# Kernel optimization log

Measured on AMD Instinct MI355X. Metric: run time of the kernel, lower is better.

## Reference

```python
import jax, jax.numpy as jnp
import numpy as np

D_MODEL = 1024
NUM_HEADS = 16
D_K = D_MODEL // NUM_HEADS
SCALE = float(np.sqrt(D_K))


def setup_inputs() -> dict:
    key = jax.random.key(0)
    ks = jax.random.split(key, 11)
    B, S, D = 2, 2048, D_MODEL
    def lin(kw):
        # xavier-uniform-ish weight, zero bias (matches torch init style)
        lim = float(np.sqrt(6.0 / (D + D)))
        return jax.random.uniform(kw, (D, D), jnp.float32, -lim, lim)
    return {
        "q": jax.random.normal(ks[0], (B, S, D), jnp.float32),
        "k": jax.random.normal(ks[1], (B, S, D), jnp.float32),
        "v": jax.random.normal(ks[2], (B, S, D), jnp.float32),
        "Wq": lin(ks[3]), "bq": jnp.zeros((D,), jnp.float32),
        "Wk": lin(ks[4]), "bk": jnp.zeros((D,), jnp.float32),
        "Wv": lin(ks[5]), "bv": jnp.zeros((D,), jnp.float32),
        "Wo": lin(ks[6]), "bo": jnp.zeros((D,), jnp.float32),
    }


def _split_heads(x):
    B, S, _ = x.shape
    return x.reshape(B, S, NUM_HEADS, D_K).transpose(0, 2, 1, 3)  # (B,H,S,dk)


def reference(q, k, v, Wq, bq, Wk, bk, Wv, bv, Wo, bo):
    # torch nn.Linear: y = x @ W.T + b
    Q = _split_heads(q @ Wq.T + bq)
    K = _split_heads(k @ Wk.T + bk)
    V = _split_heads(v @ Wv.T + bv)
    scores = jnp.einsum("bhqd,bhkd->bhqk", Q, K) / SCALE
    # numerically-stable softmax with detached max (as in the torch code)
    m = jax.lax.stop_gradient(jnp.max(scores, axis=-1, keepdims=True))
    exp_scores = jnp.exp(scores - m)
    attn = exp_scores / (jnp.sum(exp_scores, axis=-1, keepdims=True) + 1e-9)
    out = jnp.einsum("bhqk,bhkd->bhqd", attn, V)  # (B,H,S,dk)
    B, H, S, dk = out.shape
    out = out.transpose(0, 2, 1, 3).reshape(B, S, H * dk)
    return out @ Wo.T + bo
```

## Files before the change

kernel.cpp:

```cpp
#include <hip/hip_runtime.h>


#define D_MODEL 1024
#define NHEADS  16
#define DKH     64
#define SEQ     2048
#define BATCH   2
#define MTOT    (BATCH * SEQ)
#define XE      ((long)MTOT * D_MODEL)
#define WE      ((long)D_MODEL * D_MODEL)
#define QSCALE  0.18033688011112042f

typedef __attribute__((ext_vector_type(8))) short short8v;
typedef __attribute__((ext_vector_type(4))) short short4v;
typedef __attribute__((ext_vector_type(4))) float f32x4;

typedef __attribute__((address_space(1))) void as1_void;
typedef __attribute__((address_space(3))) void as3_void;

__device__ __forceinline__ void gload16(const void* g, void* l) {
    __builtin_amdgcn_global_load_lds((const as1_void*)g, (as3_void*)l, 16, 0, 0);
}

__device__ __forceinline__ unsigned short f2bf(float x) {
    unsigned int u = __float_as_uint(x);
    u += 0x7FFFu + ((u >> 16) & 1u);
    return (unsigned short)(u >> 16);
}

__device__ __forceinline__ float fexp2(float x) {
    return __builtin_amdgcn_exp2f(x);
}

__device__ __forceinline__ unsigned int cvt_pk_bf16(float lo, float hi) {
    unsigned int r;
    asm("v_cvt_pk_bf16_f32 %0, %1, %2" : "=v"(r) : "v"(lo), "v"(hi));
    return r;
}

__device__ __forceinline__ int swz_u(int row, int col) {
    int byte = (col << 1) ^ ((row & 7) << 4);
    return (row << 6) + (byte >> 1);
}

__device__ __forceinline__ int swz_v(int d, int kv) {
    int slot = (d & 6) | ((d >> 3) & 1);
    int byte = (kv << 1) ^ (slot << 4);
    return (d << 6) + (byte >> 1);
}

struct ConvArgs {
    const float*    src[7];
    unsigned short* dst[7];
    int             n4[7];
};

__global__ __launch_bounds__(256) void convert_kernel(ConvArgs a) {
    int z = blockIdx.y;
    const float4*   s = (const float4*)a.src[z];
    unsigned short* d = a.dst[z];
    int n = a.n4[z];
    for (int i = blockIdx.x * blockDim.x + threadIdx.x; i < n;
         i += gridDim.x * blockDim.x) {
        float4 v = s[i];
        ushort4 o;
        o.x = f2bf(v.x); o.y = f2bf(v.y); o.z = f2bf(v.z); o.w = f2bf(v.w);
        *(ushort4*)(d + 4L * i) = o;
    }
}

#define PBM 256
#define PBK 64
#define PTILE (PBM * PBK)

__global__ __launch_bounds__(512) void proj_kernel(
    const unsigned short* __restrict__ xb, const unsigned short* __restrict__ wb,
    const float* __restrict__ bq, const float* __restrict__ bk,
    const float* __restrict__ bv, unsigned short* __restrict__ qkv) {
    __shared__ unsigned short As[2 * PTILE];
    __shared__ unsigned short Bs[2 * PTILE];

    const int t    = threadIdx.x;
    const int lane = t & 63;
    const int w    = t >> 6;
    const int wm   = w >> 2, wn = w & 3;
    const int l15  = lane & 15, g = lane >> 4;

    const int bid = blockIdx.x;
    const int xcd = bid & 7;
    const int k   = bid >> 3;
    const int ty  = (xcd << 1) | (k & 1);
    const int tx  = (k >> 1) & 3;
    const int z   = k >> 3;
    const float* bias = (z == 0) ? bq : (z == 1) ? bk : bv;
    const float scale = (z == 0) ? QSCALE : 1.0f;

    const unsigned short* A  = xb + (long)z * XE;
    const unsigned short* Bm = wb + (long)z * WE;
    unsigned short*       C  = qkv + (long)z * XE;
    const long m0 = (long)ty * PBM;
    const long n0 = (long)tx * PBM;
    const int  K  = D_MODEL;

    f32x4 acc[8][4] = {};

    int srow[4], scol[4];
#pragma unroll
    for (int c = 0; c < 4; ++c) {
        int idx = t + c * 512;
        srow[c] = idx >> 3;
        scol[c] = ((idx & 7) ^ (srow[c] & 7)) * 8;
    }

#define PSTAGE(k0, buf)                                                    \
    _Pragma("unroll")                                                      \
    for (int c = 0; c < 4; ++c) {                                          \
        int idx = t + c * 512;                                             \
        gload16(A  + (m0 + srow[c]) * K + (k0) + scol[c],                  \
                &As[(buf) * PTILE + idx * 8]);                             \
        gload16(Bm + (n0 + srow[c]) * K + (k0) + scol[c],                  \
                &Bs[(buf) * PTILE + idx * 8]);                             \
    }

    PSTAGE(0, 0);
    int cur = 0;

    for (int it = 0; it < K / PBK; ++it) {
        const int nxt = cur ^ 1;
        const int kn  = ((it + 1) * PBK) & (K - 1);
        PSTAGE(kn, nxt);
        asm volatile("s_waitcnt vmcnt(8)" ::: "memory");
        asm volatile("s_waitcnt lgkmcnt(0)" ::: "memory");
        __builtin_amdgcn_sched_barrier(0);
        __builtin_amdgcn_s_barrier();
        __builtin_amdgcn_sched_barrier(0);

        const unsigned short* Ab = &As[cur * PTILE];
        const unsigned short* Bb = &Bs[cur * PTILE];

#pragma unroll
        for (int kk = 0; kk < 2; ++kk) {
            short8v bf_[4];
#pragma unroll
            for (int nf = 0; nf < 4; ++nf) {
                int r = wn * 64 + nf * 16 + l15;
                bf_[nf] = *(const short8v*)&Bb[r * 64 + (((kk * 4 + g) ^ (r & 7)) * 8)];
            }
#pragma unroll
            for (int mh = 0; mh < 2; ++mh) {
                short8v af_[4];
#pragma unroll
                for (int i = 0; i < 4; ++i) {
                    int r = wm * 128 + (mh * 4 + i) * 16 + l15;
                    af_[i] = *(const short8v*)&Ab[r * 64 + (((kk * 4 + g) ^ (r & 7)) * 8)];
                }
                __builtin_amdgcn_s_setprio(1);
#pragma unroll
                for (int i = 0; i < 4; ++i)
#pragma unroll
                    for (int nf = 0; nf < 4; ++nf)
                        acc[mh * 4 + i][nf] = __builtin_amdgcn_mfma_f32_16x16x32_bf16(
                            af_[i], bf_[nf], acc[mh * 4 + i][nf], 0, 0, 0);
                __builtin_amdgcn_s_setprio(0);
            }
        }

        asm volatile("s_waitcnt lgkmcnt(0)" ::: "memory");
        __builtin_amdgcn_sched_barrier(0);
        __builtin_amdgcn_s_barrier();
        __builtin_amdgcn_sched_barrier(0);
        cur = nxt;
    }

    float bvv[4];
#pragma unroll
    for (int nf = 0; nf < 4; ++nf)
        bvv[nf] = bias[n0 + wn * 64 + nf * 16 + l15];

#pragma unroll
    for (int mf = 0; mf < 8; ++mf)
#pragma unroll
        for (int nf = 0; nf < 4; ++nf)
#pragma unroll
            for (int r = 0; r < 4; ++r) {
                long row = m0 + wm * 128 + mf * 16 + g * 4 + r;
                long col = n0 + wn * 64 + nf * 16 + l15;
                C[row * (long)D_MODEL + col] =
                    f2bf((acc[mf][nf][r] + bvv[nf]) * scale);
            }
#undef PSTAGE
}

__global__ __launch_bounds__(256) void out_kernel(
    const unsigned short* __restrict__ ob, const unsigned short* __restrict__ wo,
    const float* __restrict__ bo, float* __restrict__ out) {
    __shared__ unsigned short As[128 * 32];
    __shared__ unsigned short Bs[128 * 32];

    const int t    = threadIdx.x;
    const int lane = t & 63;
    const int w    = t >> 6;
    const int wm   = w >> 1, wn = w & 1;
    const int l15  = lane & 15, g = lane >> 4;

    const int bid = blockIdx.x;
    const int xcd = bid & 7;
    const int k   = bid >> 3;
    const long m0 = (long)((xcd << 2) | (k & 3)) * 128;
    const long n0 = (long)(k >> 2) * 128;
    const int  K  = D_MODEL, N = D_MODEL;

    f32x4 acc[4][4] = {};

    const int idx0 = t, idx1 = t + 256;
    const int r0 = idx0 >> 2, c0 = (idx0 & 3) * 8;
    const int r1 = idx1 >> 2, c1 = (idx1 & 3) * 8;
    const unsigned short* pa0 = ob + (m0 + r0) * K + c0;
    const unsigned short* pa1 = ob + (m0 + r1) * K + c1;
    const unsigned short* pb0 = wo + (n0 + r0) * K + c0;
    const unsigned short* pb1 = wo + (n0 + r1) * K + c1;

    for (int k0 = 0; k0 < K; k0 += 32) {
        gload16(pa0 + k0, &As[idx0 * 8]);
        gload16(pa1 + k0, &As[idx1 * 8]);
        gload16(pb0 + k0, &Bs[idx0 * 8]);
        gload16(pb1 + k0, &Bs[idx1 * 8]);
        __syncthreads();

        short8v af[4], bf_[4];
#pragma unroll
        for (int mf = 0; mf < 4; ++mf)
            af[mf] = *(const short8v*)&As[(wm * 64 + mf * 16 + l15) * 32 + g * 8];
#pragma unroll
        for (int nf = 0; nf < 4; ++nf)
            bf_[nf] = *(const short8v*)&Bs[(wn * 64 + nf * 16 + l15) * 32 + g * 8];
#pragma unroll
        for (int mf = 0; mf < 4; ++mf)
#pragma unroll
            for (int nf = 0; nf < 4; ++nf)
                acc[mf][nf] = __builtin_amdgcn_mfma_f32_16x16x32_bf16(
                    af[mf], bf_[nf], acc[mf][nf], 0, 0, 0);
        __syncthreads();
    }

    float bvv[4];
#pragma unroll
    for (int nf = 0; nf < 4; ++nf)
        bvv[nf] = bo[n0 + wn * 64 + nf * 16 + l15];

#pragma unroll
    for (int mf = 0; mf < 4; ++mf)
#pragma unroll
        for (int nf = 0; nf < 4; ++nf)
#pragma unroll
            for (int r = 0; r < 4; ++r) {
                long row = m0 + wm * 64 + mf * 16 + g * 4 + r;
                long col = n0 + wn * 64 + nf * 16 + l15;
                out[row * (long)N + col] = acc[mf][nf][r] + bvv[nf];
            }
}

#define KVB 4096

__global__ __launch_bounds__(512) void attn_kernel(
    const unsigned short* __restrict__ Qb, const unsigned short* __restrict__ Kb,
    const unsigned short* __restrict__ Vb, unsigned short* __restrict__ Ob) {
    __shared__ alignas(16) unsigned short Ks[2 * KVB];
    __shared__ alignas(16) unsigned short Vt[2 * KVB];
    __shared__ alignas(16) unsigned short Ps[8][16 * 64];
    __shared__ alignas(16) float corrS[8][16];

    const int t = threadIdx.x, lane = t & 63, w = t >> 6;
    const int l15 = lane & 15, g = lane >> 4;
    const int bid = blockIdx.x;
    const int xcd = bid & 7;
    const int kk2 = bid >> 3;
    const int bh  = (xcd << 2) | (kk2 & 3);
    const int qb  = kk2 >> 2;
    const long headoff = (long)(bh >> 4) * SEQ * D_MODEL + (long)(bh & 15) * DKH;
    const int q0w = qb * 128 + w * 16;

    short8v qf[2];
#pragma unroll
    for (int ks = 0; ks < 2; ++ks)
        qf[ks] = *(const short8v*)(Qb + headoff +
            (long)(q0w + l15) * D_MODEL + ks * 32 + g * 8);

    short8v onesv;
#pragma unroll
    for (int j = 0; j < 8; ++j) onesv[j] = (short)0x3F80;

    f32x4 o[4] = {};
    f32x4 ol = {};
    float mrun = -3.0e38f;

    const int vd0  = (t & 31) * 2;
    const int vkv0 = (t >> 5) * 4;
    const int kr0 = t >> 3, ks0 = t & 7;

    unsigned int va[4];

#define ISSUE_V(kt)                                                        \
    _Pragma("unroll")                                                      \
    for (int j = 0; j < 4; ++j)                                            \
        va[j] = *(const unsigned int*)(Vb + headoff +                      \
            (long)((kt) + vkv0 + j) * D_MODEL + vd0);

#define ISSUE_K(kt, off)                                                   \
    gload16(Kb + headoff + (long)((kt) + kr0) * D_MODEL +                  \
                ((ks0 ^ (kr0 & 7)) << 3), &Ks[(off) + t * 8]);

#define WRITE_V(off)                                                       \
    {                                                                      \
        short4v ra, rb;                                                    \
        _Pragma("unroll")                                                  \
        for (int j = 0; j < 4; ++j) {                                      \
            ra[j] = (short)(va[j] & 0xffffu);                              \
            rb[j] = (short)(va[j] >> 16);                                  \
        }                                                                  \
        *(short4v*)&Vt[(off) + swz_v(vd0,     vkv0)] = ra;                 \
        *(short4v*)&Vt[(off) + swz_v(vd0 + 1, vkv0)] = rb;                 \
    }

    asm volatile("s_waitcnt vmcnt(0)" ::: "memory");
    ISSUE_V(0);
    ISSUE_K(0, 0);
    WRITE_V(0);
    int cur = 0;

    for (int it = 0; it < SEQ / 64; ++it) {
        const int nxt = cur ^ 1;
        const int ktn = (((it + 1) & (SEQ / 64 - 1))) * 64;
        ISSUE_V(ktn);
        ISSUE_K(ktn, nxt * KVB);
        asm volatile("s_waitcnt vmcnt(5)" ::: "memory");
        asm volatile("s_waitcnt lgkmcnt(0)" ::: "memory");
        __builtin_amdgcn_sched_barrier(0);
        __builtin_amdgcn_s_barrier();
        __builtin_amdgcn_sched_barrier(0);

        const int kO = cur * KVB;

        f32x4 st[4] = {};
        __builtin_amdgcn_s_setprio(1);
#pragma unroll
        for (int ks = 0; ks < 2; ++ks)
#pragma unroll
            for (int mf = 0; mf < 4; ++mf) {
                short8v kf = *(const short8v*)&Ks[kO + swz_u(mf * 16 + l15, ks * 32 + g * 8)];
                st[mf] = __builtin_amdgcn_mfma_f32_16x16x32_bf16(
                    kf, qf[ks], st[mf], 0, 0, 0);
            }
        __builtin_amdgcn_s_setprio(0);

        float vmax = st[0][0];
#pragma unroll
        for (int mf = 0; mf < 4; ++mf)
#pragma unroll
            for (int r = 0; r < 4; ++r)
                vmax = fmaxf(vmax, st[mf][r]);
        vmax = fmaxf(vmax, __shfl_xor(vmax, 16));
        vmax = fmaxf(vmax, __shfl_xor(vmax, 32));

        const bool grow = __any(vmax > mrun + 8.0f);
        if (grow) {
            float mnew = fmaxf(mrun, vmax);
            float corr = fexp2(mrun - mnew);
            mrun = mnew;
            if (g == 0) corrS[w][l15] = corr;
        }

#pragma unroll
        for (int mf = 0; mf < 4; ++mf)
#pragma unroll
            for (int r = 0; r < 4; ++r)
                st[mf][r] = fexp2(st[mf][r] - mrun);

        unsigned short* Pw = Ps[w];
#pragma unroll
        for (int mf = 0; mf < 4; ++mf) {
            uint2 pk;
            pk.x = cvt_pk_bf16(st[mf][0], st[mf][1]);
            pk.y = cvt_pk_bf16(st[mf][2], st[mf][3]);
            *(uint2*)&Pw[swz_u(l15, mf * 16 + g * 4)] = pk;
        }

        if (grow) {
            float4 cv = *(const float4*)&corrS[w][g * 4];
#pragma unroll
            for (int nd = 0; nd < 4; ++nd)
#pragma unroll
                for (int r = 0; r < 4; ++r)
                    o[nd][r] *= cv[r];
#pragma unroll
            for (int r = 0; r < 4; ++r) ol[r] *= cv[r];
        }

        __builtin_amdgcn_s_setprio(1);
#pragma unroll
        for (int ks2 = 0; ks2 < 2; ++ks2) {
            short8v pf = *(const short8v*)&Pw[swz_u(l15, ks2 * 32 + g * 8)];
            ol = __builtin_amdgcn_mfma_f32_16x16x32_bf16(
                pf, onesv, ol, 0, 0, 0);
#pragma unroll
            for (int nd = 0; nd < 4; ++nd) {
                short8v vf = *(const short8v*)&Vt[kO + swz_v(nd * 16 + l15, ks2 * 32 + g * 8)];
                o[nd] = __builtin_amdgcn_mfma_f32_16x16x32_bf16(
                    pf, vf, o[nd], 0, 0, 0);
            }
        }
        __builtin_amdgcn_s_setprio(0);

        WRITE_V(nxt * KVB);
        cur = nxt;
    }

#pragma unroll
    for (int r = 0; r < 4; ++r) {
        float inv = 1.f / (ol[r] + 1e-9f);
        long rowoff = headoff + (long)(q0w + g * 4 + r) * D_MODEL;
#pragma unroll
        for (int nd = 0; nd < 4; ++nd)
            Ob[rowoff + nd * 16 + l15] = f2bf(o[nd][r] * inv);
    }
#undef ISSUE_V
#undef ISSUE_K
#undef WRITE_V
}

extern "C" void kernel_launch(void* const* d_in, const int* in_sizes, int n_in,
                              void* d_out, int out_size, void* d_ws, size_t ws_size,
                              hipStream_t stream) {
    unsigned short* ws  = (unsigned short*)d_ws;
    unsigned short* xb  = ws;
    unsigned short* wb  = ws + 3L * XE;
    unsigned short* qkv = ws + 3L * XE + 4L * WE;
    unsigned short* ob  = qkv + 3L * XE;

    ConvArgs ca;
    ca.src[0] = (const float*)d_in[0]; ca.dst[0] = xb;           ca.n4[0] = (int)(XE / 4);
    ca.src[1] = (const float*)d_in[1]; ca.dst[1] = xb + XE;      ca.n4[1] = (int)(XE / 4);
    ca.src[2] = (const float*)d_in[2]; ca.dst[2] = xb + 2L * XE; ca.n4[2] = (int)(XE / 4);
    ca.src[3] = (const float*)d_in[3]; ca.dst[3] = wb;           ca.n4[3] = (int)(WE / 4);
    ca.src[4] = (const float*)d_in[5]; ca.dst[4] = wb + WE;      ca.n4[4] = (int)(WE / 4);
    ca.src[5] = (const float*)d_in[7]; ca.dst[5] = wb + 2L * WE; ca.n4[5] = (int)(WE / 4);
    ca.src[6] = (const float*)d_in[9]; ca.dst[6] = wb + 3L * WE; ca.n4[6] = (int)(WE / 4);

    hipLaunchKernelGGL(convert_kernel, dim3(512, 7), dim3(256), 0, stream, ca);

    hipLaunchKernelGGL(proj_kernel, dim3(192), dim3(512), 0, stream,
                       xb, wb, (const float*)d_in[4], (const float*)d_in[6],
                       (const float*)d_in[8], qkv);

    hipLaunchKernelGGL(attn_kernel, dim3(512), dim3(512), 0, stream,
                       qkv, qkv + XE, qkv + 2L * XE, ob);

    hipLaunchKernelGGL(out_kernel, dim3(256), dim3(256), 0, stream,
                       ob, wb + 3L * WE, (const float*)d_in[10], (float*)d_out);
}
```

Measured before the change: 132.7 us.

## Fuse fp32-to-bf16 activation conversion into projection GEMM staging

The projection kernel now reads the fp32 q/k/v activations directly, converts them to bf16 in registers and stores them to shared memory. This replaces the separate conversion pass over the three activation tensors, which wrote a bf16 copy to the workspace. The separate pass shrinks to weight conversion only. In exchange, the A-tile loads go through registers instead of async global-to-LDS loads, which doubles the A-side bytes read per tile and adds register pressure and load latency inside the main loop. The vmcnt wait is lowered to match the smaller number of async loads.

```diff
diff --git a/kernel.cpp b/kernel.cpp
--- a/kernel.cpp
+++ b/kernel.cpp
@@ -50,9 +50,9 @@
 }
 
 struct ConvArgs {
-    const float*    src[7];
-    unsigned short* dst[7];
-    int             n4[7];
+    const float*    src[4];
+    unsigned short* dst[4];
+    int             n4[4];
 };
 
 __global__ __launch_bounds__(256) void convert_kernel(ConvArgs a) {
@@ -74,7 +74,8 @@
 #define PTILE (PBM * PBK)
 
 __global__ __launch_bounds__(512) void proj_kernel(
-    const unsigned short* __restrict__ xb, const unsigned short* __restrict__ wb,
+    const float* __restrict__ xq, const float* __restrict__ xk,
+    const float* __restrict__ xv, const unsigned short* __restrict__ wb,
     const float* __restrict__ bq, const float* __restrict__ bk,
     const float* __restrict__ bv, unsigned short* __restrict__ qkv) {
     __shared__ unsigned short As[2 * PTILE];
@@ -95,7 +96,7 @@
     const float* bias = (z == 0) ? bq : (z == 1) ? bk : bv;
     const float scale = (z == 0) ? QSCALE : 1.0f;
 
-    const unsigned short* A  = xb + (long)z * XE;
+    const float* Af = (z == 0) ? xq : (z == 1) ? xk : xv;
     const unsigned short* Bm = wb + (long)z * WE;
     unsigned short*       C  = qkv + (long)z * XE;
     const long m0 = (long)ty * PBM;
@@ -113,13 +114,30 @@
     }
 
 #define PSTAGE(k0, buf)                                                    \
-    _Pragma("unroll")                                                      \
-    for (int c = 0; c < 4; ++c) {                                          \
-        int idx = t + c * 512;                                             \
-        gload16(A  + (m0 + srow[c]) * K + (k0) + scol[c],                  \
-                &As[(buf) * PTILE + idx * 8]);                             \
-        gload16(Bm + (n0 + srow[c]) * K + (k0) + scol[c],                  \
-                &Bs[(buf) * PTILE + idx * 8]);                             \
+    {                                                                      \
+        float4 a0_[4], a1_[4];                                             \
+        _Pragma("unroll")                                                  \
+        for (int c = 0; c < 4; ++c) {                                      \
+            const float* src = Af + (m0 + srow[c]) * K + (k0) + scol[c];   \
+            a0_[c] = *(const float4*)(src);                                \
+            a1_[c] = *(const float4*)(src + 4);                            \
+        }                                                                  \
+        _Pragma("unroll")                                                  \
+        for (int c = 0; c < 4; ++c) {                                      \
+            int idx = t + c * 512;                                         \
+            gload16(Bm + (n0 + srow[c]) * K + (k0) + scol[c],              \
+                    &Bs[(buf) * PTILE + idx * 8]);                         \
+        }                                                                  \
+        _Pragma("unroll")                                                  \
+        for (int c = 0; c < 4; ++c) {                                      \
+            int idx = t + c * 512;                                         \
+            uint4 pk;                                                      \
+            pk.x = cvt_pk_bf16(a0_[c].x, a0_[c].y);                        \
+            pk.y = cvt_pk_bf16(a0_[c].z, a0_[c].w);                        \
+            pk.z = cvt_pk_bf16(a1_[c].x, a1_[c].y);                        \
+            pk.w = cvt_pk_bf16(a1_[c].z, a1_[c].w);                        \
+            *(uint4*)&As[(buf) * PTILE + idx * 8] = pk;                    \
+        }                                                                  \
     }
 
     PSTAGE(0, 0);
@@ -129,7 +147,7 @@
         const int nxt = cur ^ 1;
         const int kn  = ((it + 1) * PBK) & (K - 1);
         PSTAGE(kn, nxt);
-        asm volatile("s_waitcnt vmcnt(8)" ::: "memory");
+        asm volatile("s_waitcnt vmcnt(4)" ::: "memory");
         asm volatile("s_waitcnt lgkmcnt(0)" ::: "memory");
         __builtin_amdgcn_sched_barrier(0);
         __builtin_amdgcn_s_barrier();
@@ -432,24 +450,22 @@
                               void* d_out, int out_size, void* d_ws, size_t ws_size,
                               hipStream_t stream) {
     unsigned short* ws  = (unsigned short*)d_ws;
-    unsigned short* xb  = ws;
-    unsigned short* wb  = ws + 3L * XE;
-    unsigned short* qkv = ws + 3L * XE + 4L * WE;
+    unsigned short* wb  = ws;
+    unsigned short* qkv = ws + 4L * WE;
     unsigned short* ob  = qkv + 3L * XE;
 
     ConvArgs ca;
-    ca.src[0] = (const float*)d_in[0]; ca.dst[0] = xb;           ca.n4[0] = (int)(XE / 4);
-    ca.src[1] = (const float*)d_in[1]; ca.dst[1] = xb + XE;      ca.n4[1] = (int)(XE / 4);
-    ca.src[2] = (const float*)d_in[2]; ca.dst[2] = xb + 2L * XE; ca.n4[2] = (int)(XE / 4);
-    ca.src[3] = (const float*)d_in[3]; ca.dst[3] = wb;           ca.n4[3] = (int)(WE / 4);
-    ca.src[4] = (const float*)d_in[5]; ca.dst[4] = wb + WE;      ca.n4[4] = (int)(WE / 4);
-    ca.src[5] = (const float*)d_in[7]; ca.dst[5] = wb + 2L * WE; ca.n4[5] = (int)(WE / 4);
-    ca.src[6] = (const float*)d_in[9]; ca.dst[6] = wb + 3L * WE; ca.n4[6] = (int)(WE / 4);
-
-    hipLaunchKernelGGL(convert_kernel, dim3(512, 7), dim3(256), 0, stream, ca);
+    ca.src[0] = (const float*)d_in[3]; ca.dst[0] = wb;           ca.n4[0] = (int)(WE / 4);
+    ca.src[1] = (const float*)d_in[5]; ca.dst[1] = wb + WE;      ca.n4[1] = (int)(WE / 4);
+    ca.src[2] = (const float*)d_in[7]; ca.dst[2] = wb + 2L * WE; ca.n4[2] = (int)(WE / 4);
+    ca.src[3] = (const float*)d_in[9]; ca.dst[3] = wb + 3L * WE; ca.n4[3] = (int)(WE / 4);
+
+    hipLaunchKernelGGL(convert_kernel, dim3(512, 4), dim3(256), 0, stream, ca);
 
     hipLaunchKernelGGL(proj_kernel, dim3(192), dim3(512), 0, stream,
-                       xb, wb, (const float*)d_in[4], (const float*)d_in[6],
+                       (const float*)d_in[0], (const float*)d_in[1],
+                       (const float*)d_in[2], wb,
+                       (const float*)d_in[4], (const float*)d_in[6],
                        (const float*)d_in[8], qkv);
 
     hipLaunchKernelGGL(attn_kernel, dim3(512), dim3(512), 0, stream,
```

Result: slower. 136.1 us (+2.6%).
